# Performance work log

Hardware: AMD Instinct MI355X
Metric: run time of the kernel (lower is better)

The kernel has to match this reference:

```python
import jax, jax.numpy as jnp
import numpy as np

N_EMB = 1024
HEAD_SIZE = 128


def setup_inputs() -> dict:
    key = jax.random.key(0)
    k1, k2, k3, k4 = jax.random.split(key, 4)
    B, T = 8, 4096
    x = jax.random.normal(k1, (B, T, N_EMB), dtype=jnp.float32)
    # nn.Linear(n_emb, head_size, bias=False) weights have shape [head_size, n_emb]
    s = 1.0 / np.sqrt(N_EMB)
    Wq = jax.random.uniform(k2, (HEAD_SIZE, N_EMB), jnp.float32, -s, s)
    Wk = jax.random.uniform(k3, (HEAD_SIZE, N_EMB), jnp.float32, -s, s)
    Wv = jax.random.uniform(k4, (HEAD_SIZE, N_EMB), jnp.float32, -s, s)
    return {"x": x, "Wq": Wq, "Wk": Wk, "Wv": Wv}


def reference(x, Wq, Wk, Wv):
    # x: [B, T, C]; W*: [H, C]
    B, T, C = x.shape
    H = Wq.shape[0]
    q = jnp.einsum('btc,hc->bth', x, Wq)
    k = jnp.einsum('btc,hc->bth', x, Wk)
    v = jnp.einsum('btc,hc->bth', x, Wv)
    scale = H ** -0.5
    wei = jnp.einsum('bth,bsh->bts', q, k) * scale  # [B, T, T]
    # causal mask: position t attends to s <= t
    causal = jnp.arange(T)[:, None] >= jnp.arange(T)[None, :]
    wei = jnp.where(causal, wei, -jnp.inf)
    wei = jax.nn.softmax(wei, axis=-1)
    # dropout treated as identity (eval mode)
    out = jnp.einsum('bts,bsh->bth', wei, v)  # [B, T, H]
    return out
```

## Files before the change

kernel.cpp:

```cpp
#include <hip/hip_runtime.h>
#include <hip/hip_bf16.h>

typedef __bf16 bf16_t;
typedef __attribute__((ext_vector_type(8))) __bf16 bf16x8;
typedef __attribute__((ext_vector_type(4))) __bf16 bf16x4;
typedef __attribute__((ext_vector_type(4))) float f32x4;

#define MFMA16(a, b, c) __builtin_amdgcn_mfma_f32_16x16x32_bf16((a), (b), (c), 0, 0, 0)

__device__ __forceinline__ void gload_lds16(const void* g, void* l) {
    __builtin_amdgcn_global_load_lds(
        (const __attribute__((address_space(1))) void*)g,
        (__attribute__((address_space(3))) void*)l, 16, 0, 0);
}

__global__ __launch_bounds__(256, 3) void proj_qkv(
    const float* __restrict__ X,
    const float* __restrict__ W0, const float* __restrict__ W1, const float* __restrict__ W2,
    bf16_t* __restrict__ O0, bf16_t* __restrict__ O1, bf16_t* __restrict__ O2)
{
    __shared__ __align__(16) char As[128 * 128];
    __shared__ __align__(16) char Bs[128 * 128];

    const int tid = threadIdx.x;
    const int wid = tid >> 6;
    const int lane = tid & 63;
    const int l15 = lane & 15, l4 = lane >> 4;
    const int wr = wid >> 1, wc = wid & 1;
    const int m0 = blockIdx.x * 128;

    const float* W = (blockIdx.y == 0) ? W0 : (blockIdx.y == 1 ? W1 : W2);

    const int r0 = tid >> 4;
    const int kq = tid & 15;
    const int swz = ((r0 & 7) << 4);

    f32x4 acc[4][4] = {};
    float4 xr[8];

    #pragma unroll
    for (int i = 0; i < 8; ++i)
        xr[i] = *(const float4*)(X + (size_t)(m0 + r0 + i * 16) * 1024 + kq * 4);

    for (int ks = 0; ks < 16; ++ks) {
        const int kb = ks * 64;
        #pragma unroll
        for (int i = 0; i < 8; ++i) {
            const int r = r0 + i * 16;
            bf16x4 av; av[0] = (bf16_t)xr[i].x; av[1] = (bf16_t)xr[i].y;
            av[2] = (bf16_t)xr[i].z; av[3] = (bf16_t)xr[i].w;
            *(bf16x4*)(As + r * 128 + ((kq * 8) ^ swz)) = av;
        }
        #pragma unroll
        for (int i = 0; i < 8; ++i) {
            const int r = r0 + i * 16;
            float4 wa = *(const float4*)(W + (size_t)r * 1024 + kb + kq * 4);
            bf16x4 wv; wv[0] = (bf16_t)wa.x; wv[1] = (bf16_t)wa.y;
            wv[2] = (bf16_t)wa.z; wv[3] = (bf16_t)wa.w;
            *(bf16x4*)(Bs + r * 128 + ((kq * 8) ^ swz)) = wv;
        }
        __syncthreads();
        if (ks < 15) {
            #pragma unroll
            for (int i = 0; i < 8; ++i)
                xr[i] = *(const float4*)(X + (size_t)(m0 + r0 + i * 16) * 1024 + kb + 64 + kq * 4);
        }
        #pragma unroll
        for (int kk = 0; kk < 64; kk += 32) {
            const int kbyte = 2 * kk + 16 * l4;
            bf16x8 af[4], bfr[4];
            #pragma unroll
            for (int mi = 0; mi < 4; ++mi) {
                int r = wr * 64 + mi * 16 + l15;
                af[mi] = *(const bf16x8*)(As + r * 128 + (kbyte ^ ((r & 7) << 4)));
            }
            #pragma unroll
            for (int ni = 0; ni < 4; ++ni) {
                int r = wc * 64 + ni * 16 + l15;
                bfr[ni] = *(const bf16x8*)(Bs + r * 128 + (kbyte ^ ((r & 7) << 4)));
            }
            #pragma unroll
            for (int mi = 0; mi < 4; ++mi)
                #pragma unroll
                for (int ni = 0; ni < 4; ++ni)
                    acc[mi][ni] = MFMA16(af[mi], bfr[ni], acc[mi][ni]);
        }
        __syncthreads();
    }

    if (blockIdx.y < 2) {
        const float sc = (blockIdx.y == 0) ? 0.12751754816f : 1.0f;
        bf16_t* O = (blockIdx.y == 0) ? O0 : O1;
        #pragma unroll
        for (int mi = 0; mi < 4; ++mi)
            #pragma unroll
            for (int ni = 0; ni < 4; ++ni) {
                int row = m0 + wr * 64 + mi * 16 + l4 * 4;
                int col = wc * 64 + ni * 16 + l15;
                #pragma unroll
                for (int r = 0; r < 4; ++r)
                    O[(size_t)(row + r) * 128 + col] = (bf16_t)(acc[mi][ni][r] * sc);
            }
    } else {
        #pragma unroll
        for (int mi = 0; mi < 4; ++mi)
            #pragma unroll
            for (int ni = 0; ni < 4; ++ni) {
                int row0 = m0 + wr * 64 + mi * 16 + l4 * 4;
                int col = wc * 64 + ni * 16 + l15;
                int bb = row0 >> 12, t0 = row0 & 4095;
                bf16x4 pk;
                #pragma unroll
                for (int r = 0; r < 4; ++r) pk[r] = (bf16_t)acc[mi][ni][r];
                *(bf16x4*)(O2 + ((size_t)bb << 19) + (size_t)col * 4096 + t0) = pk;
            }
    }
}

__global__ __launch_bounds__(512, 2) void attn_fwd(
    const bf16_t* __restrict__ Qb, const bf16_t* __restrict__ Kb,
    const bf16_t* __restrict__ Vtg, float* __restrict__ out, int Bn)
{
    __shared__ __align__(16) char lds[147456];

    const int tid = threadIdx.x, wid = tid >> 6, lane = tid & 63;
    const int l15 = lane & 15, l4 = lane >> 4;
    const int qh = wid >> 1, pair = wid & 1;

    const int blk = blockIdx.x;
    const int b = blk % Bn;
    const int j = blk / Bn;

    const size_t base = (size_t)b * 4096 * 128;
    const size_t baseVT = (size_t)b << 19;

    char* Pw = lds + 131072 + wid * 2048;
    const int key = l15 & 7;

    bf16x8 aones;
    #pragma unroll
    for (int e = 0; e < 8; ++e) aones[e] = (bf16_t)1.0f;

    for (int seg = 0; seg < 2; ++seg) {
        const int p = seg ? (63 - j) : j;
        const int q0 = p << 6;
        const int T = p + 1;
        const int smax = (T + 1) >> 1;
        const int qg = q0 + 16 * qh + l15;

        bf16x8 aq[4];
        #pragma unroll
        for (int kf = 0; kf < 4; ++kf)
            aq[kf] = *(const bf16x8*)(Qb + base + (size_t)qg * 128 + 32 * kf + 8 * l4);

        float mx = -1e30f;
        f32x4 ls_acc = (f32x4){0.f, 0.f, 0.f, 0.f};
        f32x4 o[8] = {};

        auto stage = [&](int s) {
            const int lt = 2 * s + pair;
            if (lt >= T) return;
            const int kv0 = lt << 6;
            if (qh < 2) {
                char* Kd = lds + pair * 32768 + (s & 1) * 16384;
                #pragma unroll
                for (int c = 0; c < 8; ++c) {
                    const int it = qh * 8 + c;
                    const int row = it * 4 + (lane >> 4);
                    const bf16_t* src = Kb + base + (size_t)(kv0 + row) * 128
                                        + (((lane & 15) ^ (row & 7)) << 3);
                    gload_lds16(src, Kd + it * 1024);
                }
            } else {
                char* Vd = lds + 65536 + pair * 32768 + (s & 1) * 16384;
                #pragma unroll
                for (int c = 0; c < 8; ++c) {
                    const int it = (qh - 2) * 8 + c;
                    const int h = it * 8 + (lane >> 3);
                    const bf16_t* src = Vtg + baseVT + (size_t)h * 4096 + kv0
                                        + (((lane & 7) ^ ((lane >> 3) & 7)) << 3);
                    gload_lds16(src, Vd + it * 1024);
                }
            }
        };

        __syncthreads();
        stage(0);
        __syncthreads();

        for (int s = 0; s < smax; ++s) {
            if (s + 1 < smax) stage(s + 1);
            const int lt = 2 * s + pair;
            if (lt < T) {
                const int kv0 = lt << 6;
                char* Kbuf = lds + pair * 32768 + (s & 1) * 16384;
                char* Vbuf = lds + 65536 + pair * 32768 + (s & 1) * 16384;

                f32x4 sa[4];
                #pragma unroll
                for (int ni = 0; ni < 4; ++ni) sa[ni] = (f32x4){0.f, 0.f, 0.f, 0.f};
                __builtin_amdgcn_s_setprio(1);
                #pragma unroll
                for (int kf = 0; kf < 4; ++kf)
                    #pragma unroll
                    for (int ni = 0; ni < 4; ++ni) {
                        bf16x8 ak = *(const bf16x8*)(Kbuf + (16 * ni + l15) * 256
                                                     + (((4 * kf + l4) ^ key) << 4));
                        sa[ni] = MFMA16(ak, aq[kf], sa[ni]);
                    }
                __builtin_amdgcn_s_setprio(0);

                if (lt == T - 1) {
                    #pragma unroll
                    for (int ni = 0; ni < 4; ++ni)
                        #pragma unroll
                        for (int r = 0; r < 4; ++r)
                            if (kv0 + 16 * ni + 4 * l4 + r > qg) sa[ni][r] = -1e30f;
                }

                float tm = -1e30f;
                #pragma unroll
                for (int ni = 0; ni < 4; ++ni)
                    tm = fmaxf(tm, fmaxf(fmaxf(sa[ni][0], sa[ni][1]),
                                         fmaxf(sa[ni][2], sa[ni][3])));
                if (__any(tm > mx + 8.0f)) {
                    tm = fmaxf(tm, __shfl_xor(tm, 16, 64));
                    tm = fmaxf(tm, __shfl_xor(tm, 32, 64));
                    const float mnew = fmaxf(mx, tm);
                    const float c = exp2f(mx - mnew);
                    ls_acc[0] *= c; ls_acc[1] *= c; ls_acc[2] *= c; ls_acc[3] *= c;
                    #pragma unroll
                    for (int mf = 0; mf < 8; ++mf) {
                        f32x4 t = o[mf];
                        t[0] *= c; t[1] *= c; t[2] *= c; t[3] *= c;
                        o[mf] = t;
                    }
                    mx = mnew;
                }
                #pragma unroll
                for (int ni = 0; ni < 4; ++ni) {
                    bf16x4 pv;
                    #pragma unroll
                    for (int r = 0; r < 4; ++r)
                        pv[r] = (bf16_t)exp2f(sa[ni][r] - mx);
                    *(bf16x4*)(Pw + l15 * 128
                               + (((2 * ni + (l4 >> 1)) ^ key) << 4) + 8 * (l4 & 1)) = pv;
                }

                __builtin_amdgcn_s_setprio(1);
                #pragma unroll
                for (int kfp = 0; kfp < 2; ++kfp) {
                    const int cb = ((4 * kfp + l4) ^ key) << 4;
                    bf16x8 pb = *(const bf16x8*)(Pw + l15 * 128 + cb);
                    ls_acc = MFMA16(aones, pb, ls_acc);
                    #pragma unroll
                    for (int mf = 0; mf < 8; ++mf) {
                        bf16x8 av = *(const bf16x8*)(Vbuf + (16 * mf + l15) * 128 + cb);
                        o[mf] = MFMA16(av, pb, o[mf]);
                    }
                }
                __builtin_amdgcn_s_setprio(0);
            }
            __syncthreads();
        }

        if (pair == 1) {
            char* dst = lds + qh * 8192;
            #pragma unroll
            for (int mf = 0; mf < 8; ++mf)
                *(f32x4*)(dst + mf * 1024 + lane * 16) = o[mf];
            *(float2*)(lds + 65536 + qh * 512 + lane * 8) = make_float2(mx, ls_acc[0]);
        }
        __syncthreads();
        if (pair == 0) {
            float2 st = *(const float2*)(lds + 65536 + qh * 512 + lane * 8);
            const float mB = st.x, lB = st.y;
            const float M = fmaxf(mx, mB);
            const float a = exp2f(mx - M), b2 = exp2f(mB - M);
            const float linv = 1.f / (ls_acc[0] * a + lB * b2);
            char* srcO = lds + qh * 8192;
            float* op = out + ((size_t)b * 4096 + qg) * 128 + 4 * l4;
            #pragma unroll
            for (int mf = 0; mf < 8; ++mf) {
                f32x4 ob = *(const f32x4*)(srcO + mf * 1024 + lane * 16);
                f32x4 r;
                #pragma unroll
                for (int e = 0; e < 4; ++e) r[e] = (o[mf][e] * a + ob[e] * b2) * linv;
                *(f32x4*)(op + 16 * mf) = r;
            }
        }
    }
}

extern "C" void kernel_launch(void* const* d_in, const int* in_sizes, int n_in,
                              void* d_out, int out_size, void* d_ws, size_t ws_size,
                              hipStream_t stream) {
    const float* X  = (const float*)d_in[0];
    const float* Wq = (const float*)d_in[1];
    const float* Wk = (const float*)d_in[2];
    const float* Wv = (const float*)d_in[3];
    float* out = (float*)d_out;

    const int M = in_sizes[0] / 1024;
    const int Bn = M / 4096;

    bf16_t* Qb  = (bf16_t*)d_ws;
    bf16_t* KbP = Qb + (size_t)M * 128;
    bf16_t* VtP = KbP + (size_t)M * 128;

    proj_qkv<<<dim3(M / 128, 3), 256, 0, stream>>>(X, Wq, Wk, Wv, Qb, KbP, VtP);
    attn_fwd<<<dim3(32 * Bn), 512, 0, stream>>>(Qb, KbP, VtP, out, Bn);
}
```

Baseline: 119.7 us.

## Fuse Q, K, V projections into one block per row tile

The projection kernel now computes all three Q, K and V outputs in one block per 128-row tile, using a 384-wide weight tile in LDS and 512 threads. Previously each of the three grid rows reloaded and converted the same fp32 X tile, so X was read from memory three times; now it is read once. The trade-off is a smaller grid with fewer, larger blocks and more accumulator registers per thread, which may reduce latency hiding.

```diff
diff --git a/kernel.cpp b/kernel.cpp
--- a/kernel.cpp
+++ b/kernel.cpp
@@ -14,107 +14,104 @@
         (__attribute__((address_space(3))) void*)l, 16, 0, 0);
 }
 
-__global__ __launch_bounds__(256, 3) void proj_qkv(
+__global__ __launch_bounds__(512, 2) void proj_qkv(
     const float* __restrict__ X,
     const float* __restrict__ W0, const float* __restrict__ W1, const float* __restrict__ W2,
     bf16_t* __restrict__ O0, bf16_t* __restrict__ O1, bf16_t* __restrict__ O2)
 {
     __shared__ __align__(16) char As[128 * 128];
-    __shared__ __align__(16) char Bs[128 * 128];
+    __shared__ __align__(16) char Bs[384 * 128];
 
     const int tid = threadIdx.x;
     const int wid = tid >> 6;
     const int lane = tid & 63;
     const int l15 = lane & 15, l4 = lane >> 4;
-    const int wr = wid >> 1, wc = wid & 1;
+    const int wr = wid >> 1;
+    const int wc = wid & 1;
     const int m0 = blockIdx.x * 128;
-
-    const float* W = (blockIdx.y == 0) ? W0 : (blockIdx.y == 1 ? W1 : W2);
 
     const int r0 = tid >> 4;
     const int kq = tid & 15;
-    const int swz = ((r0 & 7) << 4);
-
-    f32x4 acc[4][4] = {};
-    float4 xr[8];
+
+    f32x4 acc[2][12] = {};
+    float4 xr[4];
 
     #pragma unroll
-    for (int i = 0; i < 8; ++i)
-        xr[i] = *(const float4*)(X + (size_t)(m0 + r0 + i * 16) * 1024 + kq * 4);
+    for (int i = 0; i < 4; ++i)
+        xr[i] = *(const float4*)(X + (size_t)(m0 + r0 + 32 * i) * 1024 + kq * 4);
 
     for (int ks = 0; ks < 16; ++ks) {
         const int kb = ks * 64;
         #pragma unroll
-        for (int i = 0; i < 8; ++i) {
-            const int r = r0 + i * 16;
+        for (int i = 0; i < 4; ++i) {
+            const int r = r0 + 32 * i;
             bf16x4 av; av[0] = (bf16_t)xr[i].x; av[1] = (bf16_t)xr[i].y;
             av[2] = (bf16_t)xr[i].z; av[3] = (bf16_t)xr[i].w;
-            *(bf16x4*)(As + r * 128 + ((kq * 8) ^ swz)) = av;
-        }
-        #pragma unroll
-        for (int i = 0; i < 8; ++i) {
-            const int r = r0 + i * 16;
-            float4 wa = *(const float4*)(W + (size_t)r * 1024 + kb + kq * 4);
+            *(bf16x4*)(As + r * 128 + ((kq * 8) ^ ((r & 7) << 4))) = av;
+        }
+        #pragma unroll
+        for (int i = 0; i < 12; ++i) {
+            const int r = r0 + 32 * i;
+            const float* Wp = (i < 4) ? W0 : (i < 8 ? W1 : W2);
+            const int wrow = r0 + 32 * (i & 3);
+            float4 wa = *(const float4*)(Wp + (size_t)wrow * 1024 + kb + kq * 4);
             bf16x4 wv; wv[0] = (bf16_t)wa.x; wv[1] = (bf16_t)wa.y;
             wv[2] = (bf16_t)wa.z; wv[3] = (bf16_t)wa.w;
-            *(bf16x4*)(Bs + r * 128 + ((kq * 8) ^ swz)) = wv;
+            *(bf16x4*)(Bs + r * 128 + ((kq * 8) ^ ((r & 7) << 4))) = wv;
         }
         __syncthreads();
         if (ks < 15) {
             #pragma unroll
-            for (int i = 0; i < 8; ++i)
-                xr[i] = *(const float4*)(X + (size_t)(m0 + r0 + i * 16) * 1024 + kb + 64 + kq * 4);
+            for (int i = 0; i < 4; ++i)
+                xr[i] = *(const float4*)(X + (size_t)(m0 + r0 + 32 * i) * 1024 + kb + 64 + kq * 4);
         }
         #pragma unroll
         for (int kk = 0; kk < 64; kk += 32) {
             const int kbyte = 2 * kk + 16 * l4;
-            bf16x8 af[4], bfr[4];
-            #pragma unroll
-            for (int mi = 0; mi < 4; ++mi) {
-                int r = wr * 64 + mi * 16 + l15;
+            bf16x8 af[2], bfr[12];
+            #pragma unroll
+            for (int mi = 0; mi < 2; ++mi) {
+                int r = wr * 32 + mi * 16 + l15;
                 af[mi] = *(const bf16x8*)(As + r * 128 + (kbyte ^ ((r & 7) << 4)));
             }
             #pragma unroll
-            for (int ni = 0; ni < 4; ++ni) {
-                int r = wc * 64 + ni * 16 + l15;
+            for (int ni = 0; ni < 12; ++ni) {
+                int r = wc * 192 + ni * 16 + l15;
                 bfr[ni] = *(const bf16x8*)(Bs + r * 128 + (kbyte ^ ((r & 7) << 4)));
             }
             #pragma unroll
-            for (int mi = 0; mi < 4; ++mi)
-                #pragma unroll
-                for (int ni = 0; ni < 4; ++ni)
+            for (int mi = 0; mi < 2; ++mi)
+                #pragma unroll
+                for (int ni = 0; ni < 12; ++ni)
                     acc[mi][ni] = MFMA16(af[mi], bfr[ni], acc[mi][ni]);
         }
         __syncthreads();
     }
 
-    if (blockIdx.y < 2) {
-        const float sc = (blockIdx.y == 0) ? 0.12751754816f : 1.0f;
-        bf16_t* O = (blockIdx.y == 0) ? O0 : O1;
-        #pragma unroll
-        for (int mi = 0; mi < 4; ++mi)
-            #pragma unroll
-            for (int ni = 0; ni < 4; ++ni) {
-                int row = m0 + wr * 64 + mi * 16 + l4 * 4;
-                int col = wc * 64 + ni * 16 + l15;
+    const float qs = 0.12751754816f;
+    #pragma unroll
+    for (int mi = 0; mi < 2; ++mi)
+        #pragma unroll
+        for (int ni = 0; ni < 12; ++ni) {
+            const int gcol = 192 * wc + 16 * ni + l15;
+            const int sel = gcol >> 7, lc = gcol & 127;
+            const int row = m0 + 32 * wr + 16 * mi + 4 * l4;
+            if (sel == 0) {
                 #pragma unroll
                 for (int r = 0; r < 4; ++r)
-                    O[(size_t)(row + r) * 128 + col] = (bf16_t)(acc[mi][ni][r] * sc);
-            }
-    } else {
-        #pragma unroll
-        for (int mi = 0; mi < 4; ++mi)
-            #pragma unroll
-            for (int ni = 0; ni < 4; ++ni) {
-                int row0 = m0 + wr * 64 + mi * 16 + l4 * 4;
-                int col = wc * 64 + ni * 16 + l15;
-                int bb = row0 >> 12, t0 = row0 & 4095;
+                    O0[(size_t)(row + r) * 128 + lc] = (bf16_t)(acc[mi][ni][r] * qs);
+            } else if (sel == 1) {
+                #pragma unroll
+                for (int r = 0; r < 4; ++r)
+                    O1[(size_t)(row + r) * 128 + lc] = (bf16_t)acc[mi][ni][r];
+            } else {
+                const int bb = row >> 12, t0 = row & 4095;
                 bf16x4 pk;
                 #pragma unroll
                 for (int r = 0; r < 4; ++r) pk[r] = (bf16_t)acc[mi][ni][r];
-                *(bf16x4*)(O2 + ((size_t)bb << 19) + (size_t)col * 4096 + t0) = pk;
-            }
-    }
+                *(bf16x4*)(O2 + ((size_t)bb << 19) + (size_t)lc * 4096 + t0) = pk;
+            }
+        }
 }
 
 __global__ __launch_bounds__(512, 2) void attn_fwd(
@@ -308,6 +305,6 @@
     bf16_t* KbP = Qb + (size_t)M * 128;
     bf16_t* VtP = KbP + (size_t)M * 128;
 
-    proj_qkv<<<dim3(M / 128, 3), 256, 0, stream>>>(X, Wq, Wk, Wv, Qb, KbP, VtP);
+    proj_qkv<<<dim3(M / 128), 512, 0, stream>>>(X, Wq, Wk, Wv, Qb, KbP, VtP);
     attn_fwd<<<dim3(32 * Bn), 512, 0, stream>>>(Qb, KbP, VtP, out, Bn);
 }
```

Measured after the change: 124.6 us. +4.1%, slower.
